# Performance work log

Hardware: AMD Instinct MI355X
Metric: run time of the kernel (lower is better)

## Reference

```python
import jax, jax.numpy as jnp
import numpy as np
import math

B, S, D, H = 8, 1024, 1024, 16
HD = D // H  # head_features = 64
SCALE = math.sqrt(HD)


def setup_inputs() -> dict:
    key = jax.random.key(0)
    k0, k1, k2, k3, k4 = jax.random.split(key, 5)
    x = jax.random.normal(k0, (B, S, D), dtype=jnp.float32)
    attn_mask = (jax.random.uniform(k1, (B, S, S)) < 0.9).astype(jnp.float32)
    w_scale = 1.0 / math.sqrt(D)  # keep unsafe exp in finite range
    Wq = jax.random.normal(k2, (D, D), dtype=jnp.float32) * w_scale
    Wk = jax.random.normal(k3, (D, D), dtype=jnp.float32) * w_scale
    Wv = jax.random.normal(k4, (D, D), dtype=jnp.float32) * w_scale
    return {"x": x, "attn_mask": attn_mask, "Wq": Wq, "Wk": Wk, "Wv": Wv}


def reference(x, attn_mask, Wq, Wk, Wv):
    b, s, _ = x.shape

    def split_heads(t):  # [b,s,D] -> [b,H,s,HD]
        return t.reshape(b, s, H, HD).transpose(0, 2, 1, 3)

    q = split_heads(x @ Wq)
    k = split_heads(x @ Wk)
    v = split_heads(x @ Wv)

    # unsafe softmax: exp without max subtraction, multiplicative mask, +1e-8 denom
    scores = jnp.einsum('bhsd,bhtd->bhst', q, k) / SCALE
    e = jnp.exp(scores) * attn_mask[:, None, :, :]
    w = e / (e.sum(axis=3, keepdims=True) + 1e-8)

    ctx = jnp.einsum('bhst,bhtd->bhsd', w, v)  # [b,H,s,HD]
    return ctx.transpose(0, 2, 1, 3).reshape(b, s, D)
```

## Files before the change

### kernel.cpp

```cpp
#include <hip/hip_runtime.h>

#define KDIM 1024

typedef _Float16 half8 __attribute__((ext_vector_type(8)));
typedef _Float16 half4 __attribute__((ext_vector_type(4)));
typedef __fp16 fp16x2 __attribute__((ext_vector_type(2)));
typedef __fp16 fp16x4 __attribute__((ext_vector_type(4)));
typedef float f32x4 __attribute__((ext_vector_type(4)));

#if defined(__has_builtin)
#if __has_builtin(__builtin_amdgcn_global_load_lds)
#define HAVE_GLDS 1
#endif
#if __has_builtin(__builtin_amdgcn_exp2f)
#define EXP2(x) __builtin_amdgcn_exp2f(x)
#endif
#if __has_builtin(__builtin_amdgcn_cvt_pkrtz)
#define HAVE_PKRTZ 1
#endif
#if __has_builtin(__builtin_amdgcn_fdot2)
#define HAVE_FDOT2 1
#endif
#endif
#ifndef EXP2
#define EXP2(x) exp2f(x)
#endif

__device__ __forceinline__ void stage16(const _Float16* g, _Float16* wave_base, int lane) {
#ifdef HAVE_GLDS
  __builtin_amdgcn_global_load_lds(
      (const __attribute__((address_space(1))) void*)g,
      (__attribute__((address_space(3))) void*)wave_base, 16, 0, 0);
#else
  *(half8*)(wave_base + lane * 8) = *(const half8*)g;
#endif
}

__global__ void cast_x_kernel(const float* __restrict__ x, _Float16* __restrict__ xb) {
  size_t i = ((size_t)blockIdx.x * 256 + threadIdx.x) * 4;
  float4 v = *(const float4*)(x + i);
  half4 h = { (_Float16)v.x, (_Float16)v.y, (_Float16)v.z, (_Float16)v.w };
  *(half4*)(xb + i) = h;
}

__global__ void wtrans_kernel(const float* __restrict__ Wq, const float* __restrict__ Wk,
                              const float* __restrict__ Wv, _Float16* __restrict__ Wqkvt) {
  int z = blockIdx.z;
  const float* src = z == 0 ? Wq : (z == 1 ? Wk : Wv);
  _Float16* dst = Wqkvt + (size_t)z * KDIM * KDIM;
  float sc = (z == 0) ? 0.18033688011112042f : 1.0f;
  __shared__ _Float16 tile[32][33];
  int tx = threadIdx.x & 31, ty = threadIdx.x >> 5;
  int c0 = blockIdx.x * 32, r0 = blockIdx.y * 32;
#pragma unroll
  for (int i = 0; i < 4; i++) {
    int r = r0 + ty + i * 8;
    tile[tx][ty + i * 8] = (_Float16)(src[(size_t)r * KDIM + c0 + tx] * sc);
  }
  __syncthreads();
#pragma unroll
  for (int i = 0; i < 4; i++) {
    int n = c0 + ty + i * 8;
    dst[(size_t)n * KDIM + r0 + tx] = tile[ty + i * 8][tx];
  }
}

__global__ void maskbits_kernel(const float* __restrict__ m, unsigned long long* __restrict__ bits) {
  size_t i = (size_t)blockIdx.x * 256 + threadIdx.x;
  unsigned long long b = __ballot(m[i] != 0.0f);
  if ((threadIdx.x & 63) == 0) bits[i >> 6] = b;
}

__global__ __launch_bounds__(256, 2)
void gemm_kernel(const _Float16* __restrict__ A, const _Float16* __restrict__ Bt,
                 _Float16* __restrict__ Qt, _Float16* __restrict__ Kh,
                 _Float16* __restrict__ Vth) {
  __shared__ _Float16 As[128 * 32];
  __shared__ _Float16 Bs[128 * 32];
  int tid = threadIdx.x;
  int lane = tid & 63, w4 = tid >> 6;
  int la = lane & 15, qd = lane >> 4;
  int wm = w4 & 1, wn = w4 >> 1;
  int m0 = blockIdx.y * 128, n0 = blockIdx.x * 128;
  int r = tid >> 2, c = (tid & 3) * 8;
  const _Float16* Ag = A + (size_t)(m0 + r) * KDIM + c;
  const _Float16* Bg = Bt + (size_t)(n0 + r) * KDIM + c;
  _Float16* a0 = As + w4 * 512;
  _Float16* b0 = Bs + w4 * 512;
  f32x4 acc[4][4] = {};
  for (int kt = 0; kt < KDIM; kt += 32) {
    stage16(Ag + kt, a0, lane);
    stage16(Ag + (size_t)64 * KDIM + kt, a0 + 2048, lane);
    stage16(Bg + kt, b0, lane);
    stage16(Bg + (size_t)64 * KDIM + kt, b0 + 2048, lane);
    __syncthreads();
    half8 af[4], bf[4];
#pragma unroll
    for (int mi = 0; mi < 4; mi++)
      af[mi] = *(const half8*)(As + (wm * 64 + mi * 16 + la) * 32 + qd * 8);
#pragma unroll
    for (int ni = 0; ni < 4; ni++)
      bf[ni] = *(const half8*)(Bs + (wn * 64 + ni * 16 + la) * 32 + qd * 8);
#pragma unroll
    for (int mi = 0; mi < 4; mi++)
#pragma unroll
      for (int ni = 0; ni < 4; ni++)
        acc[mi][ni] = __builtin_amdgcn_mfma_f32_16x16x32_f16(af[mi], bf[ni], acc[mi][ni], 0, 0, 0);
    __syncthreads();
  }
  int which = n0 >> 10;
  int hh = ((n0 + wn * 64) >> 6) & 15;
  int mbase = m0 + wm * 64;
  int b = mbase >> 10, s0 = mbase & 1023;
  if (which == 1) {
#pragma unroll
    for (int mi = 0; mi < 4; mi++)
#pragma unroll
      for (int ni = 0; ni < 4; ni++) {
        f32x4 v = acc[mi][ni];
        int s = s0 + mi * 16 + qd * 4;
        int d = ni * 16 + la;
#pragma unroll
        for (int rg = 0; rg < 4; rg++)
          Kh[(((size_t)(b * 16 + hh)) * 1024 + s + rg) * 64 + d] = (_Float16)v[rg];
      }
  } else {
    _Float16* dst = (which == 0) ? Qt : Vth;
    _Float16* ep = (w4 < 2) ? (As + w4 * 2048) : (Bs + (w4 - 2) * 2048);
    _Float16* base = dst + ((size_t)(b * 16 + hh)) * 64 * 1024;
    int rr = lane >> 2, c4 = lane & 3;
#pragma unroll
    for (int ni = 0; ni < 4; ni++) {
#pragma unroll
      for (int mi = 0; mi < 4; mi++) {
        f32x4 v = acc[mi][ni];
        half4 hv = { (_Float16)v[0], (_Float16)v[1], (_Float16)v[2], (_Float16)v[3] };
        *(half4*)(ep + la * 72 + mi * 16 + qd * 4) = hv;
      }
      half8 o0 = *(const half8*)(ep + rr * 72 + c4 * 16);
      half8 o1 = *(const half8*)(ep + rr * 72 + c4 * 16 + 8);
      _Float16* gp = base + (size_t)(ni * 16 + rr) * 1024 + s0 + c4 * 16;
      *(half8*)gp = o0;
      *(half8*)(gp + 8) = o1;
    }
  }
}

__global__ __launch_bounds__(512, 2)
void attn_kernel(const _Float16* __restrict__ Qt, const _Float16* __restrict__ K,
                 const _Float16* __restrict__ Vt, const unsigned long long* __restrict__ mbits,
                 float* __restrict__ out) {
  __shared__ _Float16 Ks[2 * 64 * 32];
  __shared__ _Float16 Vs[2 * 64 * 40];
  int tid = threadIdx.x;
  int lane = tid & 63, w4 = tid >> 6;
  int la = lane & 15, qd = lane >> 4;
  int linear = blockIdx.x;
  int xlo = linear & 7;
  int tmp = linear >> 3;
  int qt = tmp & 3;
  int hb = (tmp >> 2) * 8 + xlo;
  int h = hb & 15, b = hb >> 4;
  const _Float16* Qp = Qt + (size_t)hb * 64 * 1024;
  const _Float16* Kp = K + (size_t)hb * 1024 * 64;
  const _Float16* Vp = Vt + (size_t)hb * 64 * 1024;
  int q0w = qt * 256 + w4 * 16;
  half8 qf[2][2];
#pragma unroll
  for (int qi = 0; qi < 2; qi++)
#pragma unroll
    for (int ks = 0; ks < 2; ks++)
#pragma unroll
      for (int j = 0; j < 8; j++)
        qf[qi][ks][j] = Qp[(size_t)(ks * 32 + qd * 8 + j) * 1024 + q0w + qi * 128 + la];
  unsigned long long mq[2][4];
#pragma unroll
  for (int qi = 0; qi < 2; qi++) {
    const ulonglong2* mp =
        (const ulonglong2*)(mbits + ((size_t)b * 1024 + q0w + qi * 128 + la) * 16 + qd * 4);
    ulonglong2 m01 = mp[0];
    ulonglong2 m23 = mp[1];
    mq[qi][0] = m01.x; mq[qi][1] = m01.y; mq[qi][2] = m23.x; mq[qi][3] = m23.y;
  }
  f32x4 acco[2][4] = {};
  float rs[2] = {0.f, 0.f};
  int kt_t = (tid & 255) >> 2;
  int kt_d = (tid >> 8) * 32 + (tid & 3) * 8;
  _Float16* kbase = Ks + w4 * 512;
  int vd = tid >> 3;
  int vt = (tid & 7) * 8;
  _Float16* vdst = Vs + (vt >= 32 ? 2560 : 0) + vd * 40 + (vt & 31);
#if defined(HAVE_FDOT2) && defined(HAVE_PKRTZ)
  fp16x2 one2 = { (__fp16)1.0f, (__fp16)1.0f };
#endif
  for (int tt = 0; tt < 16; tt++) {
    half8 vv = *(const half8*)(Vp + (size_t)vd * 1024 + tt * 64 + vt);
    stage16(Kp + (size_t)(tt * 64 + kt_t) * 64 + kt_d, kbase, lane);
    *(half8*)vdst = vv;
    __syncthreads();
    unsigned long long mw0 = __shfl(mq[0][tt & 3], ((tt >> 2) << 4) + la);
    unsigned long long mw1 = __shfl(mq[1][tt & 3], ((tt >> 2) << 4) + la);
#pragma unroll
    for (int tsub = 0; tsub < 4; tsub++) {
      half8 kf0 = *(const half8*)(Ks + (tsub * 16 + la) * 32 + qd * 8);
      half8 kf1 = *(const half8*)(Ks + 2048 + (tsub * 16 + la) * 32 + qd * 8);
      f32x4 a0 = {}, a1 = {};
      a0 = __builtin_amdgcn_mfma_f32_16x16x32_f16(kf0, qf[0][0], a0, 0, 0, 0);
      a1 = __builtin_amdgcn_mfma_f32_16x16x32_f16(kf0, qf[1][0], a1, 0, 0, 0);
      a0 = __builtin_amdgcn_mfma_f32_16x16x32_f16(kf1, qf[0][1], a0, 0, 0, 0);
      a1 = __builtin_amdgcn_mfma_f32_16x16x32_f16(kf1, qf[1][1], a1, 0, 0, 0);
      half4 pf[2];
#pragma unroll
      for (int qi = 0; qi < 2; qi++) {
        const f32x4& aa = qi ? a1 : a0;
        unsigned long long mw = qi ? mw1 : mw0;
        float e0 = ((mw >> (tsub * 16 + qd * 4 + 0)) & 1ull) ? EXP2(aa[0]) : 0.0f;
        float e1 = ((mw >> (tsub * 16 + qd * 4 + 1)) & 1ull) ? EXP2(aa[1]) : 0.0f;
        float e2 = ((mw >> (tsub * 16 + qd * 4 + 2)) & 1ull) ? EXP2(aa[2]) : 0.0f;
        float e3 = ((mw >> (tsub * 16 + qd * 4 + 3)) & 1ull) ? EXP2(aa[3]) : 0.0f;
#ifdef HAVE_PKRTZ
        fp16x2 p01 = __builtin_amdgcn_cvt_pkrtz(e0, e1);
        fp16x2 p23 = __builtin_amdgcn_cvt_pkrtz(e2, e3);
        fp16x4 pfv = __builtin_shufflevector(p01, p23, 0, 1, 2, 3);
        pf[qi] = __builtin_bit_cast(half4, pfv);
#else
        pf[qi][0] = (_Float16)e0; pf[qi][1] = (_Float16)e1;
        pf[qi][2] = (_Float16)e2; pf[qi][3] = (_Float16)e3;
#endif
#if defined(HAVE_FDOT2) && defined(HAVE_PKRTZ)
        rs[qi] = __builtin_amdgcn_fdot2(p01, one2, rs[qi], false);
        rs[qi] = __builtin_amdgcn_fdot2(p23, one2, rs[qi], false);
#else
        rs[qi] += e0 + e1 + e2 + e3;
#endif
      }
#pragma unroll
      for (int nsub = 0; nsub < 4; nsub++) {
        half4 vf = *(const half4*)(Vs + (tsub >> 1) * 2560 + (nsub * 16 + la) * 40 +
                                   (tsub & 1) * 16 + qd * 4);
        acco[0][nsub] = __builtin_amdgcn_mfma_f32_16x16x16f16(pf[0], vf, acco[0][nsub], 0, 0, 0);
        acco[1][nsub] = __builtin_amdgcn_mfma_f32_16x16x16f16(pf[1], vf, acco[1][nsub], 0, 0, 0);
      }
    }
    __syncthreads();
  }
  float* op = out + (size_t)b * 1024 * 1024 + (size_t)h * 64;
#pragma unroll
  for (int qi = 0; qi < 2; qi++) {
    float r0 = rs[qi];
    r0 += __shfl_xor(r0, 16);
    r0 += __shfl_xor(r0, 32);
    float inv_q = 1.0f / (r0 + 1e-8f);
#pragma unroll
    for (int rg = 0; rg < 4; rg++) {
      float inv = __shfl(inv_q, qd * 4 + rg);
      int s = q0w + qi * 128 + qd * 4 + rg;
#pragma unroll
      for (int nsub = 0; nsub < 4; nsub++)
        op[(size_t)s * 1024 + nsub * 16 + la] = acco[qi][nsub][rg] * inv;
    }
  }
}

extern "C" void kernel_launch(void* const* d_in, const int* in_sizes, int n_in,
                              void* d_out, int out_size, void* d_ws, size_t ws_size,
                              hipStream_t stream) {
  (void)in_sizes; (void)n_in; (void)out_size; (void)ws_size;
  const float* x = (const float*)d_in[0];
  const float* am = (const float*)d_in[1];
  const float* Wq = (const float*)d_in[2];
  const float* Wk = (const float*)d_in[3];
  const float* Wv = (const float*)d_in[4];
  float* out = (float*)d_out;

  char* p = (char*)d_ws;
  _Float16* xb = (_Float16*)p;    p += (size_t)8192 * 1024 * 2;
  _Float16* Wqkvt = (_Float16*)p; p += (size_t)3 * 1024 * 1024 * 2;
  _Float16* Qt = (_Float16*)p;    p += (size_t)8192 * 1024 * 2;
  _Float16* Kh = (_Float16*)p;    p += (size_t)8192 * 1024 * 2;
  _Float16* Vth = (_Float16*)p;   p += (size_t)8192 * 1024 * 2;
  unsigned long long* mb = (unsigned long long*)p;

  cast_x_kernel<<<8192, 256, 0, stream>>>(x, xb);
  wtrans_kernel<<<dim3(32, 32, 3), 256, 0, stream>>>(Wq, Wk, Wv, Wqkvt);
  maskbits_kernel<<<32768, 256, 0, stream>>>(am, mb);
  gemm_kernel<<<dim3(24, 64), 256, 0, stream>>>(xb, Wqkvt, Qt, Kh, Vth);
  attn_kernel<<<512, 512, 0, stream>>>(Qt, Kh, Vth, mb, out);
}
```

Baseline: 263.4 us.

## Double-buffer K/V tiles in attention and merge prep kernels into one launch

The attention loop now uses two LDS buffers for the K and V tiles. The next tile's global loads are issued before computing on the current one, and the V store to LDS is deferred until after the MFMA work, so one barrier per iteration replaces two. Separately, the cast, weight-transpose and mask-bitpack kernels are merged into a single launch that branches on block index, which removes launch gaps. The cost is double the LDS use in attention, which may affect occupancy at 2 blocks per CU, plus extra registers to hold the prefetched V.

```diff
diff --git a/kernel.cpp b/kernel.cpp
--- a/kernel.cpp
+++ b/kernel.cpp
@@ -36,39 +36,43 @@
 #endif
 }
 
-__global__ void cast_x_kernel(const float* __restrict__ x, _Float16* __restrict__ xb) {
-  size_t i = ((size_t)blockIdx.x * 256 + threadIdx.x) * 4;
-  float4 v = *(const float4*)(x + i);
-  half4 h = { (_Float16)v.x, (_Float16)v.y, (_Float16)v.z, (_Float16)v.w };
-  *(half4*)(xb + i) = h;
-}
-
-__global__ void wtrans_kernel(const float* __restrict__ Wq, const float* __restrict__ Wk,
-                              const float* __restrict__ Wv, _Float16* __restrict__ Wqkvt) {
-  int z = blockIdx.z;
-  const float* src = z == 0 ? Wq : (z == 1 ? Wk : Wv);
-  _Float16* dst = Wqkvt + (size_t)z * KDIM * KDIM;
-  float sc = (z == 0) ? 0.18033688011112042f : 1.0f;
+__global__ void prep_kernel(const float* __restrict__ x, const float* __restrict__ am,
+                            const float* __restrict__ Wq, const float* __restrict__ Wk,
+                            const float* __restrict__ Wv, _Float16* __restrict__ xb,
+                            _Float16* __restrict__ Wqkvt, unsigned long long* __restrict__ bits) {
   __shared__ _Float16 tile[32][33];
-  int tx = threadIdx.x & 31, ty = threadIdx.x >> 5;
-  int c0 = blockIdx.x * 32, r0 = blockIdx.y * 32;
-#pragma unroll
-  for (int i = 0; i < 4; i++) {
-    int r = r0 + ty + i * 8;
-    tile[tx][ty + i * 8] = (_Float16)(src[(size_t)r * KDIM + c0 + tx] * sc);
-  }
-  __syncthreads();
-#pragma unroll
-  for (int i = 0; i < 4; i++) {
-    int n = c0 + ty + i * 8;
-    dst[(size_t)n * KDIM + r0 + tx] = tile[ty + i * 8][tx];
-  }
-}
-
-__global__ void maskbits_kernel(const float* __restrict__ m, unsigned long long* __restrict__ bits) {
-  size_t i = (size_t)blockIdx.x * 256 + threadIdx.x;
-  unsigned long long b = __ballot(m[i] != 0.0f);
-  if ((threadIdx.x & 63) == 0) bits[i >> 6] = b;
+  int bid = blockIdx.x;
+  if (bid < 8192) {
+    size_t i = ((size_t)bid * 256 + threadIdx.x) * 4;
+    float4 v = *(const float4*)(x + i);
+    half4 h = { (_Float16)v.x, (_Float16)v.y, (_Float16)v.z, (_Float16)v.w };
+    *(half4*)(xb + i) = h;
+  } else if (bid < 11264) {
+    int zz = bid - 8192;
+    int z = zz >> 10;
+    int rem = zz & 1023;
+    int bx = rem & 31, by = rem >> 5;
+    const float* src = z == 0 ? Wq : (z == 1 ? Wk : Wv);
+    _Float16* dst = Wqkvt + (size_t)z * KDIM * KDIM;
+    float sc = (z == 0) ? 0.18033688011112042f : 1.0f;
+    int tx = threadIdx.x & 31, ty = threadIdx.x >> 5;
+    int c0 = bx * 32, r0 = by * 32;
+#pragma unroll
+    for (int i = 0; i < 4; i++) {
+      int r = r0 + ty + i * 8;
+      tile[tx][ty + i * 8] = (_Float16)(src[(size_t)r * KDIM + c0 + tx] * sc);
+    }
+    __syncthreads();
+#pragma unroll
+    for (int i = 0; i < 4; i++) {
+      int n = c0 + ty + i * 8;
+      dst[(size_t)n * KDIM + r0 + tx] = tile[ty + i * 8][tx];
+    }
+  } else {
+    size_t i = (size_t)(bid - 11264) * 256 + threadIdx.x;
+    unsigned long long b = __ballot(am[i] != 0.0f);
+    if ((threadIdx.x & 63) == 0) bits[i >> 6] = b;
+  }
 }
 
 __global__ __launch_bounds__(256, 2)
@@ -150,8 +154,8 @@
 void attn_kernel(const _Float16* __restrict__ Qt, const _Float16* __restrict__ K,
                  const _Float16* __restrict__ Vt, const unsigned long long* __restrict__ mbits,
                  float* __restrict__ out) {
-  __shared__ _Float16 Ks[2 * 64 * 32];
-  __shared__ _Float16 Vs[2 * 64 * 40];
+  __shared__ _Float16 Ks[2][2 * 64 * 32];
+  __shared__ _Float16 Vs[2][2 * 64 * 40];
   int tid = threadIdx.x;
   int lane = tid & 63, w4 = tid >> 6;
   int la = lane & 15, qd = lane >> 4;
@@ -186,24 +190,33 @@
   float rs[2] = {0.f, 0.f};
   int kt_t = (tid & 255) >> 2;
   int kt_d = (tid >> 8) * 32 + (tid & 3) * 8;
-  _Float16* kbase = Ks + w4 * 512;
   int vd = tid >> 3;
   int vt = (tid & 7) * 8;
-  _Float16* vdst = Vs + (vt >= 32 ? 2560 : 0) + vd * 40 + (vt & 31);
+  int vs_off = (vt >= 32 ? 2560 : 0) + vd * 40 + (vt & 31);
 #if defined(HAVE_FDOT2) && defined(HAVE_PKRTZ)
   fp16x2 one2 = { (__fp16)1.0f, (__fp16)1.0f };
 #endif
+  {
+    stage16(Kp + (size_t)kt_t * 64 + kt_d, Ks[0] + w4 * 512, lane);
+    half8 vv = *(const half8*)(Vp + (size_t)vd * 1024 + vt);
+    *(half8*)(Vs[0] + vs_off) = vv;
+  }
+  __syncthreads();
   for (int tt = 0; tt < 16; tt++) {
-    half8 vv = *(const half8*)(Vp + (size_t)vd * 1024 + tt * 64 + vt);
-    stage16(Kp + (size_t)(tt * 64 + kt_t) * 64 + kt_d, kbase, lane);
-    *(half8*)vdst = vv;
-    __syncthreads();
+    int cur = tt & 1, nxt = cur ^ 1;
+    half8 vvn;
+    if (tt < 15) {
+      vvn = *(const half8*)(Vp + (size_t)vd * 1024 + (tt + 1) * 64 + vt);
+      stage16(Kp + (size_t)((tt + 1) * 64 + kt_t) * 64 + kt_d, Ks[nxt] + w4 * 512, lane);
+    }
+    const _Float16* ks_ = Ks[cur];
+    const _Float16* vs_ = Vs[cur];
     unsigned long long mw0 = __shfl(mq[0][tt & 3], ((tt >> 2) << 4) + la);
     unsigned long long mw1 = __shfl(mq[1][tt & 3], ((tt >> 2) << 4) + la);
 #pragma unroll
     for (int tsub = 0; tsub < 4; tsub++) {
-      half8 kf0 = *(const half8*)(Ks + (tsub * 16 + la) * 32 + qd * 8);
-      half8 kf1 = *(const half8*)(Ks + 2048 + (tsub * 16 + la) * 32 + qd * 8);
+      half8 kf0 = *(const half8*)(ks_ + (tsub * 16 + la) * 32 + qd * 8);
+      half8 kf1 = *(const half8*)(ks_ + 2048 + (tsub * 16 + la) * 32 + qd * 8);
       f32x4 a0 = {}, a1 = {};
       a0 = __builtin_amdgcn_mfma_f32_16x16x32_f16(kf0, qf[0][0], a0, 0, 0, 0);
       a1 = __builtin_amdgcn_mfma_f32_16x16x32_f16(kf0, qf[1][0], a1, 0, 0, 0);
@@ -236,12 +249,13 @@
       }
 #pragma unroll
       for (int nsub = 0; nsub < 4; nsub++) {
-        half4 vf = *(const half4*)(Vs + (tsub >> 1) * 2560 + (nsub * 16 + la) * 40 +
+        half4 vf = *(const half4*)(vs_ + (tsub >> 1) * 2560 + (nsub * 16 + la) * 40 +
                                    (tsub & 1) * 16 + qd * 4);
         acco[0][nsub] = __builtin_amdgcn_mfma_f32_16x16x16f16(pf[0], vf, acco[0][nsub], 0, 0, 0);
         acco[1][nsub] = __builtin_amdgcn_mfma_f32_16x16x16f16(pf[1], vf, acco[1][nsub], 0, 0, 0);
       }
     }
+    if (tt < 15) *(half8*)(Vs[nxt] + vs_off) = vvn;
     __syncthreads();
   }
   float* op = out + (size_t)b * 1024 * 1024 + (size_t)h * 64;
@@ -281,9 +295,7 @@
   _Float16* Vth = (_Float16*)p;   p += (size_t)8192 * 1024 * 2;
   unsigned long long* mb = (unsigned long long*)p;
 
-  cast_x_kernel<<<8192, 256, 0, stream>>>(x, xb);
-  wtrans_kernel<<<dim3(32, 32, 3), 256, 0, stream>>>(Wq, Wk, Wv, Wqkvt);
-  maskbits_kernel<<<32768, 256, 0, stream>>>(am, mb);
+  prep_kernel<<<44032, 256, 0, stream>>>(x, am, Wq, Wk, Wv, xb, Wqkvt, mb);
   gemm_kernel<<<dim3(24, 64), 256, 0, stream>>>(xb, Wqkvt, Qt, Kh, Vth);
   attn_kernel<<<512, 512, 0, stream>>>(Qt, Kh, Vth, mb, out);
 }
```

Result: faster. 251.6 us (-4.5%).
